# Kernel optimization log

Measured on AMD Instinct MI355X. Metric: run time of the kernel, lower is better.

The kernel has to match this reference:

```python
import jax, jax.numpy as jnp
import numpy as np

L = 2       # num_layers
D = 256     # d_model
DFF = 1024  # d_ffn
NH = 8      # n_heads
NP = 4      # n_points
CIN = 512   # in_channels
B = 8
HH = 64
WW = 64
EPS = 1e-5


def setup_inputs() -> dict:
    key = jax.random.key(0)
    ks = iter(jax.random.split(key, 48))
    def w(shape, s=0.02):
        return jax.random.normal(next(ks), shape, jnp.float32) * s
    inp = dict(
        x=jax.random.normal(next(ks), (B, CIN, HH, WW), jnp.float32),
        W_in=w((D, CIN)),
        bn1_g=jnp.ones((D,), jnp.float32), bn1_b=jnp.zeros((D,), jnp.float32),
        bn1_m=jnp.zeros((D,), jnp.float32), bn1_v=jnp.ones((D,), jnp.float32),
        query_embed=w((HH * WW, D), 1.0),
        Woff=w((L, D, NH * NP * 2)), boff=w((L, NH * NP * 2), 2.0),
        Wattn=w((L, D, NH * NP)), battn=jnp.zeros((L, NH * NP), jnp.float32),
        Wval=w((L, D, D)), bval=jnp.zeros((L, D), jnp.float32),
        Wo=w((L, D, D)), bo=jnp.zeros((L, D), jnp.float32),
        ln1_g=jnp.ones((L, D), jnp.float32), ln1_b=jnp.zeros((L, D), jnp.float32),
        W1=w((L, D, DFF)), b1=jnp.zeros((L, DFF), jnp.float32),
        W2=w((L, DFF, D)), b2=jnp.zeros((L, D), jnp.float32),
        ln2_g=jnp.ones((L, D), jnp.float32), ln2_b=jnp.zeros((L, D), jnp.float32),
        W_out=w((CIN, D)),
        bn2_g=jnp.ones((CIN,), jnp.float32), bn2_b=jnp.zeros((CIN,), jnp.float32),
        bn2_m=jnp.zeros((CIN,), jnp.float32), bn2_v=jnp.ones((CIN,), jnp.float32),
    )
    return inp


def layer_norm(x, g, b):
    m = jnp.mean(x, axis=-1, keepdims=True)
    v = jnp.mean((x - m) ** 2, axis=-1, keepdims=True)
    return (x - m) * jax.lax.rsqrt(v + EPS) * g + b


def bilinear_sample(value, loc, Hh, Ww):
    # value: (B, NH, dh, H*W); loc: (B, Lq, NH, NP, 2) normalized to [0,1]
    # Matches F.grid_sample(align_corners=False, padding_mode='zeros') with grid=2*loc-1.
    Bn, Lq, nH, P, _ = loc.shape
    gx = loc[..., 0] * Ww - 0.5
    gy = loc[..., 1] * Hh - 0.5
    x0 = jnp.floor(gx)
    y0 = jnp.floor(gy)
    wx = gx - x0
    wy = gy - y0
    x0i = x0.astype(jnp.int32)
    y0i = y0.astype(jnp.int32)

    def t(a):  # (B,Lq,NH,P) -> (B,NH,1,Lq*P)
        return jnp.transpose(a, (0, 2, 1, 3)).reshape(Bn, nH, 1, Lq * P)

    def gather(xi, yi):
        valid = (xi >= 0) & (xi < Ww) & (yi >= 0) & (yi < Hh)
        xc = jnp.clip(xi, 0, Ww - 1)
        yc = jnp.clip(yi, 0, Hh - 1)
        idx = t(yc * Ww + xc)  # (B,NH,1,Lq*P)
        v = jnp.take_along_axis(value, idx, axis=3)  # (B,NH,dh,Lq*P)
        return v * t(valid).astype(value.dtype)

    v00 = gather(x0i, y0i)
    v10 = gather(x0i + 1, y0i)
    v01 = gather(x0i, y0i + 1)
    v11 = gather(x0i + 1, y0i + 1)
    wxt = t(wx)
    wyt = t(wy)
    out = (v00 * (1 - wxt) * (1 - wyt) + v10 * wxt * (1 - wyt)
           + v01 * (1 - wxt) * wyt + v11 * wxt * wyt)
    return out.reshape(Bn, nH, -1, Lq, P)  # (B,NH,dh,Lq,NP)


def reference(x, W_in, bn1_g, bn1_b, bn1_m, bn1_v, query_embed,
              Woff, boff, Wattn, battn, Wval, bval, Wo, bo,
              ln1_g, ln1_b, W1, b1, W2, b2, ln2_g, ln2_b,
              W_out, bn2_g, bn2_b, bn2_m, bn2_v):
    Bn, C, Hh, Ww = x.shape
    HW = Hh * Ww
    dh = D // NH

    # proj_in: 1x1 conv (no bias) + BN (inference) + ReLU
    xp = jnp.einsum('bchw,dc->bdhw', x, W_in)
    xp = (xp - bn1_m[:, None, None]) * jax.lax.rsqrt(bn1_v[:, None, None] + EPS)
    xp = jax.nn.relu(xp * bn1_g[:, None, None] + bn1_b[:, None, None])
    src = xp.reshape(Bn, D, HW).transpose(0, 2, 1)  # (B, HW, D)

    # reference points: centers of pixels, normalized
    ry = (jnp.arange(Hh, dtype=jnp.float32) + 0.5) / Hh
    rx = (jnp.arange(Ww, dtype=jnp.float32) + 0.5) / Ww
    yy, xx = jnp.meshgrid(ry, rx, indexing='ij')
    refpts = jnp.stack([xx, yy], axis=-1).reshape(HW, 2)  # (HW, 2) as (x, y)
    norm = jnp.array([Ww, Hh], jnp.float32)

    q = jnp.broadcast_to(query_embed[None], (Bn, HW, D))
    for i in range(L):
        # --- MSDeformAttn (n_levels=1) ---
        val = (src @ Wval[i] + bval[i]).reshape(Bn, HW, NH, dh)
        val = val.transpose(0, 2, 3, 1)  # (B, NH, dh, HW)
        off = (q @ Woff[i] + boff[i]).reshape(Bn, HW, NH, NP, 2)
        attn = jax.nn.softmax((q @ Wattn[i] + battn[i]).reshape(Bn, HW, NH, NP), axis=-1)
        loc = refpts[None, :, None, None, :] + off / norm  # (B, HW, NH, NP, 2)
        samp = bilinear_sample(val, loc, Hh, Ww)  # (B, NH, dh, HW, NP)
        o = jnp.einsum('bhdqp,bhqp->bqhd', samp, attn.transpose(0, 2, 1, 3))
        o = o.reshape(Bn, HW, D) @ Wo[i] + bo[i]
        q = layer_norm(q + o, ln1_g[i], ln1_b[i])
        # --- FFN ---
        ffn = jax.nn.relu(q @ W1[i] + b1[i]) @ W2[i] + b2[i]
        q = layer_norm(q + ffn, ln2_g[i], ln2_b[i])

    # proj_out: 1x1 conv (no bias) + BN (inference) + ReLU
    y = q.transpose(0, 2, 1).reshape(Bn, D, Hh, Ww)
    y = jnp.einsum('bdhw,cd->bchw', y, W_out)
    y = (y - bn2_m[:, None, None]) * jax.lax.rsqrt(bn2_v[:, None, None] + EPS)
    return jax.nn.relu(y * bn2_g[:, None, None] + bn2_b[:, None, None])
```

## Files before the change

kernel.cpp:

```cpp
#include <hip/hip_runtime.h>
#include <cstdint>

#define LYR 2
#define DM  256
#define DFFN 1024
#define CINC 512
#define BBATCH 8
#define HWTOT 4096
#define EPSV 1e-5f

using u16 = unsigned short;
typedef __attribute__((ext_vector_type(8))) short bf16x8;
typedef __attribute__((ext_vector_type(4))) float f32x4;

__device__ inline u16 f2b(float v) {
    union { float f; uint32_t u; } x; x.f = v;
    uint32_t r = x.u + 0x7fffu + ((x.u >> 16) & 1u);
    return (u16)(r >> 16);
}
__device__ inline uint32_t pk2(float a, float b) {
    return (uint32_t)f2b(a) | ((uint32_t)f2b(b) << 16);
}
__device__ inline float blo(uint32_t d) {
    union { uint32_t i; float f; } x; x.i = d << 16; return x.f;
}
__device__ inline float bhi(uint32_t d) {
    union { uint32_t i; float f; } x; x.i = d & 0xffff0000u; return x.f;
}

template<int MODE>
__global__ __launch_bounds__(256) void mfma_gemm(
    const u16* __restrict__ A, const u16* __restrict__ Bt,
    const float* __restrict__ scale, const float* __restrict__ shift,
    void* __restrict__ Cv, int M, int N, int K, int ldc,
    long long a_zs, long long b_zs, long long c_zs, int swz, int gxlog)
{
    __shared__ u16 As[4][4096];
    __shared__ u16 Bs[4][4096];
    const int tid = threadIdx.x;
    const int lane = tid & 63;
    const int wid = tid >> 6;
    const int wm = (wid & 1) << 6, wn = (wid >> 1) << 6;
    const int quad = lane >> 4, r = lane & 15;

    int bx = blockIdx.x, by = blockIdx.y;
    if (swz) {
        int linear = by * gridDim.x + bx;
        int xcd = linear & 7;
        int s = linear >> 3;
        bx = s & (gridDim.x - 1);
        by = xcd * (gridDim.y >> 3) + (s >> gxlog);
    }
    const int m0 = by << 7, n0 = bx << 7;
    const u16* Ab = A + (long long)blockIdx.z * a_zs + (long long)m0 * K;
    const u16* Bb = Bt + (long long)blockIdx.z * b_zs + (long long)n0 * K;

    const int u0 = tid, u1 = tid + 256;
    const int mu0 = u0 >> 2, cu0 = (u0 & 3) ^ ((mu0 >> 1) & 3);
    const int mu1 = u1 >> 2, cu1 = (u1 & 3) ^ ((mu1 >> 1) & 3);
    const long long ga0 = (long long)mu0 * K + cu0 * 8;
    const long long ga1 = (long long)mu1 * K + cu1 * 8;

    int aoff[4], boff[4];
#pragma unroll
    for (int t = 0; t < 4; ++t) {
        int m = wm + t * 16 + r;
        aoff[t] = (m * 4 + (quad ^ ((m >> 1) & 3))) * 8;
        int n = wn + t * 16 + r;
        boff[t] = (n * 4 + (quad ^ ((n >> 1) & 3))) * 8;
    }

    f32x4 acc[4][4];
#pragma unroll
    for (int i = 0; i < 4; ++i)
#pragma unroll
        for (int j = 0; j < 4; ++j) acc[i][j] = (f32x4){0.f, 0.f, 0.f, 0.f};

    const int NT = K >> 5;

#define GSTAGE(g, b) do {                                                                       \
    const long long kk = (long long)(g) << 5;                                                   \
    __builtin_amdgcn_global_load_lds((const __attribute__((address_space(1))) void*)(Ab + ga0 + kk), \
        (__attribute__((address_space(3))) void*)(&As[b][u0 * 8]), 16, 0, 0);                   \
    __builtin_amdgcn_global_load_lds((const __attribute__((address_space(1))) void*)(Ab + ga1 + kk), \
        (__attribute__((address_space(3))) void*)(&As[b][u1 * 8]), 16, 0, 0);                   \
    __builtin_amdgcn_global_load_lds((const __attribute__((address_space(1))) void*)(Bb + ga0 + kk), \
        (__attribute__((address_space(3))) void*)(&Bs[b][u0 * 8]), 16, 0, 0);                   \
    __builtin_amdgcn_global_load_lds((const __attribute__((address_space(1))) void*)(Bb + ga1 + kk), \
        (__attribute__((address_space(3))) void*)(&Bs[b][u1 * 8]), 16, 0, 0);                   \
} while (0)

    GSTAGE(0, 0);
    GSTAGE(1, 1);
    GSTAGE(2, 2);

    for (int t = 0; t < NT; ++t) {
        if (t < NT - 2)       asm volatile("s_waitcnt vmcnt(8)" ::: "memory");
        else if (t == NT - 2) asm volatile("s_waitcnt vmcnt(4)" ::: "memory");
        else                  asm volatile("s_waitcnt vmcnt(0)" ::: "memory");
        __builtin_amdgcn_s_barrier();
        __builtin_amdgcn_sched_barrier(0);
        if (t + 3 < NT) GSTAGE(t + 3, (t + 3) & 3);
        const u16* Ap = As[t & 3];
        const u16* Bp = Bs[t & 3];
        bf16x8 af[4], bf[4];
#pragma unroll
        for (int tt = 0; tt < 4; ++tt) af[tt] = *(const bf16x8*)(Ap + aoff[tt]);
#pragma unroll
        for (int tt = 0; tt < 4; ++tt) bf[tt] = *(const bf16x8*)(Bp + boff[tt]);
#pragma unroll
        for (int i = 0; i < 4; ++i)
#pragma unroll
            for (int j = 0; j < 4; ++j)
                acc[i][j] = __builtin_amdgcn_mfma_f32_16x16x32_bf16(bf[j], af[i], acc[i][j], 0, 0, 0);
    }
#undef GSTAGE

    const long long zc = (long long)blockIdx.z * c_zs;
    float4 sh4[4], sc4[4];
    if (MODE != 3) {
#pragma unroll
        for (int j = 0; j < 4; ++j) {
            int colb = n0 + wn + j * 16 + quad * 4;
            sh4[j] = *(const float4*)&shift[colb];
            if (MODE == 1) sc4[j] = *(const float4*)&scale[colb];
        }
    }
#pragma unroll
    for (int i = 0; i < 4; ++i) {
        const int row = m0 + wm + i * 16 + r;
        float rsc = 0.f, rsh = 0.f;
        if (MODE == 3) { rsc = scale[row]; rsh = shift[row]; }
#pragma unroll
        for (int j = 0; j < 4; ++j) {
            const int colb = n0 + wn + j * 16 + quad * 4;
            f32x4 v = acc[i][j];
            if (MODE == 0) {
                uint2 o;
                o.x = pk2(v[0] + sh4[j].x, v[1] + sh4[j].y);
                o.y = pk2(v[2] + sh4[j].z, v[3] + sh4[j].w);
                *(uint2*)((u16*)Cv + zc + (long long)row * ldc + colb) = o;
            } else if (MODE == 1) {
                uint2 o;
                o.x = pk2(fmaxf(v[0] * sc4[j].x + sh4[j].x, 0.f), fmaxf(v[1] * sc4[j].y + sh4[j].y, 0.f));
                o.y = pk2(fmaxf(v[2] * sc4[j].z + sh4[j].z, 0.f), fmaxf(v[3] * sc4[j].w + sh4[j].w, 0.f));
                *(uint2*)((u16*)Cv + zc + (long long)row * ldc + colb) = o;
            } else if (MODE == 2) {
                float4 o = {v[0] + sh4[j].x, v[1] + sh4[j].y, v[2] + sh4[j].z, v[3] + sh4[j].w};
                *(float4*)((float*)Cv + zc + (long long)row * ldc + colb) = o;
            } else {
                float4 o = {fmaxf(v[0] * rsc + rsh, 0.f), fmaxf(v[1] * rsc + rsh, 0.f),
                            fmaxf(v[2] * rsc + rsh, 0.f), fmaxf(v[3] * rsc + rsh, 0.f)};
                *(float4*)((float*)Cv + zc + (long long)row * ldc + colb) = o;
            }
        }
    }
}

template<int WRITEQ, int OA>
__global__ __launch_bounds__(512, 4) void fused_layer(
    const u16* __restrict__ oms, const u16* __restrict__ woF,
    const u16* __restrict__ w1F, const u16* __restrict__ w2F,
    const u16* __restrict__ woaF,
    const float* __restrict__ bo, const float* __restrict__ b1, const float* __restrict__ b2,
    const float* __restrict__ boa1,
    float* __restrict__ q, u16* __restrict__ q16, float* __restrict__ offat,
    const float* __restrict__ g1, const float* __restrict__ be1,
    const float* __restrict__ g2, const float* __restrict__ be2)
{
    __shared__ u16 AqO[16384];
    __shared__ u16 AqQ[16384];
    __shared__ float red_s[8][64], red_ss[8][64];
    const int tid = threadIdx.x;
    const int lane = tid & 63;
    const int w = tid >> 6;
    const int quad = lane >> 4, r = lane & 15;
    const int m0 = blockIdx.x << 6;

    const u16* Ab = oms + (long long)m0 * DM;
#pragma unroll
    for (int i = 0; i < 4; ++i) {
        int u = tid + i * 512;
        int ks = u >> 8, v = u & 255;
        int m = v >> 2, c = (v & 3) ^ ((m >> 1) & 3);
        __builtin_amdgcn_global_load_lds((const __attribute__((address_space(1))) void*)(Ab + (long long)m * DM + ks * 32 + c * 8),
                                         (__attribute__((address_space(3))) void*)(AqO + u * 8), 16, 0, 0);
    }

    int aoff[4];
#pragma unroll
    for (int t = 0; t < 4; ++t) {
        int m = t * 16 + r;
        aoff[t] = (m * 4 + (quad ^ ((m >> 1) & 3))) * 8;
    }

    f32x4 acc[4][2];
#pragma unroll
    for (int i = 0; i < 4; ++i)
#pragma unroll
        for (int j = 0; j < 2; ++j) acc[i][j] = (f32x4){0.f, 0.f, 0.f, 0.f};

    __syncthreads();

#pragma unroll
    for (int ks = 0; ks < 8; ++ks) {
        const u16* bp = woF + ((size_t)(ks * 16 + 2 * w) * 64 + lane) * 8;
        bf16x8 bf0 = *(const bf16x8*)bp;
        bf16x8 bf1 = *(const bf16x8*)(bp + 512);
        bf16x8 af[4];
#pragma unroll
        for (int t = 0; t < 4; ++t) af[t] = *(const bf16x8*)(AqO + ks * 2048 + aoff[t]);
#pragma unroll
        for (int i = 0; i < 4; ++i) {
            acc[i][0] = __builtin_amdgcn_mfma_f32_16x16x32_bf16(bf0, af[i], acc[i][0], 0, 0, 0);
            acc[i][1] = __builtin_amdgcn_mfma_f32_16x16x32_bf16(bf1, af[i], acc[i][1], 0, 0, 0);
        }
    }

    float4 sh2[2];
#pragma unroll
    for (int j = 0; j < 2; ++j)
        sh2[j] = *(const float4*)&bo[w * 32 + j * 16 + quad * 4];

    float s_[4] = {0.f, 0.f, 0.f, 0.f}, ss_[4] = {0.f, 0.f, 0.f, 0.f};
#pragma unroll
    for (int i = 0; i < 4; ++i) {
        const int row = m0 + i * 16 + r;
#pragma unroll
        for (int j = 0; j < 2; ++j) {
            const int colb = w * 32 + j * 16 + quad * 4;
            float4 qo = *(const float4*)&q[(size_t)row * DM + colb];
            acc[i][j][0] += sh2[j].x + qo.x;
            acc[i][j][1] += sh2[j].y + qo.y;
            acc[i][j][2] += sh2[j].z + qo.z;
            acc[i][j][3] += sh2[j].w + qo.w;
#pragma unroll
            for (int e = 0; e < 4; ++e) {
                s_[i] += acc[i][j][e];
                ss_[i] += acc[i][j][e] * acc[i][j][e];
            }
        }
    }
#pragma unroll
    for (int i = 0; i < 4; ++i) {
        s_[i] += __shfl_xor(s_[i], 16);  ss_[i] += __shfl_xor(ss_[i], 16);
        s_[i] += __shfl_xor(s_[i], 32);  ss_[i] += __shfl_xor(ss_[i], 32);
    }
    if (quad == 0) {
#pragma unroll
        for (int i = 0; i < 4; ++i) {
            red_s[w][i * 16 + r] = s_[i];
            red_ss[w][i * 16 + r] = ss_[i];
        }
    }
    __syncthreads();

    float mean[4], rstd[4];
#pragma unroll
    for (int i = 0; i < 4; ++i) {
        float S = 0.f, SS = 0.f;
#pragma unroll
        for (int w2 = 0; w2 < 8; ++w2) { S += red_s[w2][i * 16 + r]; SS += red_ss[w2][i * 16 + r]; }
        mean[i] = S * (1.0f / 256.0f);
        rstd[i] = rsqrtf(SS * (1.0f / 256.0f) - mean[i] * mean[i] + EPSV);
    }

    f32x4 oreg[4][2];
    {
        float4 g4[2], bt4[2];
#pragma unroll
        for (int j = 0; j < 2; ++j) {
            int colb = w * 32 + j * 16 + quad * 4;
            g4[j] = *(const float4*)&g1[colb];
            bt4[j] = *(const float4*)&be1[colb];
        }
#pragma unroll
        for (int i = 0; i < 4; ++i) {
            const int mm = i * 16 + r;
#pragma unroll
            for (int j = 0; j < 2; ++j) {
                float o0 = (acc[i][j][0] - mean[i]) * rstd[i] * g4[j].x + bt4[j].x;
                float o1 = (acc[i][j][1] - mean[i]) * rstd[i] * g4[j].y + bt4[j].y;
                float o2 = (acc[i][j][2] - mean[i]) * rstd[i] * g4[j].z + bt4[j].z;
                float o3 = (acc[i][j][3] - mean[i]) * rstd[i] * g4[j].w + bt4[j].w;
                oreg[i][j] = (f32x4){o0, o1, o2, o3};
                const int pp = (j * 2 + (quad >> 1)) ^ ((r >> 1) & 3);
                *(uint2*)(AqQ + w * 2048 + (mm * 4 + pp) * 8 + (quad & 1) * 4) =
                    make_uint2(pk2(o0, o1), pk2(o2, o3));
            }
        }
    }
    __syncthreads();

    f32x4 acc2[4][2];
#pragma unroll
    for (int i = 0; i < 4; ++i)
#pragma unroll
        for (int j = 0; j < 2; ++j) acc2[i][j] = (f32x4){0.f, 0.f, 0.f, 0.f};

    for (int qq = 0; qq < 4; ++qq) {
        if (qq) __syncthreads();
#pragma unroll
        for (int j = 0; j < 2; ++j) {
            f32x4 a1[4];
#pragma unroll
            for (int i = 0; i < 4; ++i) a1[i] = (f32x4){0.f, 0.f, 0.f, 0.f};
            __builtin_amdgcn_s_setprio(1);
#pragma unroll
            for (int ks = 0; ks < 8; ++ks) {
                const u16* bp = w1F + ((size_t)(ks * 64 + qq * 16 + w * 2 + j) * 64 + lane) * 8;
                bf16x8 bf = *(const bf16x8*)bp;
                bf16x8 af[4];
#pragma unroll
                for (int t = 0; t < 4; ++t) af[t] = *(const bf16x8*)(AqQ + ks * 2048 + aoff[t]);
#pragma unroll
                for (int i = 0; i < 4; ++i)
                    a1[i] = __builtin_amdgcn_mfma_f32_16x16x32_bf16(bf, af[i], a1[i], 0, 0, 0);
            }
            __builtin_amdgcn_s_setprio(0);
            const int cb = qq * 256 + w * 32 + j * 16 + quad * 4;
            const float4 b14 = *(const float4*)&b1[cb];
            const int lane2 = r | (((j * 2 + (quad >> 1)) & 3) << 4);
            const int eo = (quad & 1) * 4;
#pragma unroll
            for (int i = 0; i < 4; ++i) {
                f32x4 v = a1[i];
                uint2 o;
                o.x = pk2(fmaxf(v[0] + b14.x, 0.f), fmaxf(v[1] + b14.y, 0.f));
                o.y = pk2(fmaxf(v[2] + b14.z, 0.f), fmaxf(v[3] + b14.w, 0.f));
                *(uint2*)(AqO + ((w * 4 + i) * 64 + lane2) * 8 + eo) = o;
            }
        }
        __syncthreads();

        __builtin_amdgcn_s_setprio(1);
#pragma unroll
        for (int ks = 0; ks < 8; ++ks) {
            const u16* bp = w2F + ((size_t)((qq * 8 + ks) * 16 + w * 2) * 64 + lane) * 8;
            bf16x8 bf0 = *(const bf16x8*)bp;
            bf16x8 bf1 = *(const bf16x8*)(bp + 512);
            bf16x8 af[4];
#pragma unroll
            for (int t = 0; t < 4; ++t) af[t] = *(const bf16x8*)(AqO + ((ks * 4 + t) * 64 + lane) * 8);
#pragma unroll
            for (int i = 0; i < 4; ++i) {
                acc2[i][0] = __builtin_amdgcn_mfma_f32_16x16x32_bf16(bf0, af[i], acc2[i][0], 0, 0, 0);
                acc2[i][1] = __builtin_amdgcn_mfma_f32_16x16x32_bf16(bf1, af[i], acc2[i][1], 0, 0, 0);
            }
        }
        __builtin_amdgcn_s_setprio(0);
    }

#pragma unroll
    for (int j = 0; j < 2; ++j)
        sh2[j] = *(const float4*)&b2[w * 32 + j * 16 + quad * 4];

#pragma unroll
    for (int i = 0; i < 4; ++i) { s_[i] = 0.f; ss_[i] = 0.f; }
#pragma unroll
    for (int i = 0; i < 4; ++i) {
#pragma unroll
        for (int j = 0; j < 2; ++j) {
            acc2[i][j][0] += sh2[j].x + oreg[i][j][0];
            acc2[i][j][1] += sh2[j].y + oreg[i][j][1];
            acc2[i][j][2] += sh2[j].z + oreg[i][j][2];
            acc2[i][j][3] += sh2[j].w + oreg[i][j][3];
#pragma unroll
            for (int e = 0; e < 4; ++e) {
                s_[i] += acc2[i][j][e];
                ss_[i] += acc2[i][j][e] * acc2[i][j][e];
            }
        }
    }
#pragma unroll
    for (int i = 0; i < 4; ++i) {
        s_[i] += __shfl_xor(s_[i], 16);  ss_[i] += __shfl_xor(ss_[i], 16);
        s_[i] += __shfl_xor(s_[i], 32);  ss_[i] += __shfl_xor(ss_[i], 32);
    }
    if (quad == 0) {
#pragma unroll
        for (int i = 0; i < 4; ++i) {
            red_s[w][i * 16 + r] = s_[i];
            red_ss[w][i * 16 + r] = ss_[i];
        }
    }
    __syncthreads();

#pragma unroll
    for (int i = 0; i < 4; ++i) {
        float S = 0.f, SS = 0.f;
#pragma unroll
        for (int w2 = 0; w2 < 8; ++w2) { S += red_s[w2][i * 16 + r]; SS += red_ss[w2][i * 16 + r]; }
        mean[i] = S * (1.0f / 256.0f);
        rstd[i] = rsqrtf(SS * (1.0f / 256.0f) - mean[i] * mean[i] + EPSV);
    }

    float4 g4[2], bt4[2];
#pragma unroll
    for (int j = 0; j < 2; ++j) {
        int colb = w * 32 + j * 16 + quad * 4;
        g4[j] = *(const float4*)&g2[colb];
        bt4[j] = *(const float4*)&be2[colb];
    }
#pragma unroll
    for (int i = 0; i < 4; ++i) {
        const int row = m0 + i * 16 + r;
#pragma unroll
        for (int j = 0; j < 2; ++j) {
            const int colb = w * 32 + j * 16 + quad * 4;
            float o0 = (acc2[i][j][0] - mean[i]) * rstd[i] * g4[j].x + bt4[j].x;
            float o1 = (acc2[i][j][1] - mean[i]) * rstd[i] * g4[j].y + bt4[j].y;
            float o2 = (acc2[i][j][2] - mean[i]) * rstd[i] * g4[j].z + bt4[j].z;
            float o3 = (acc2[i][j][3] - mean[i]) * rstd[i] * g4[j].w + bt4[j].w;
            oreg[i][j] = (f32x4){o0, o1, o2, o3};
            if (WRITEQ)
                *(float4*)&q[(size_t)row * DM + colb] = make_float4(o0, o1, o2, o3);
            *(uint2*)(q16 + (size_t)row * DM + colb) = make_uint2(pk2(o0, o1), pk2(o2, o3));
        }
    }

    if (OA) {
#pragma unroll
        for (int i = 0; i < 4; ++i) {
            const int mm = i * 16 + r;
#pragma unroll
            for (int j = 0; j < 2; ++j) {
                const int pp = (j * 2 + (quad >> 1)) ^ ((r >> 1) & 3);
                *(uint2*)(AqQ + w * 2048 + (mm * 4 + pp) * 8 + (quad & 1) * 4) =
                    make_uint2(pk2(oreg[i][j][0], oreg[i][j][1]),
                               pk2(oreg[i][j][2], oreg[i][j][3]));
            }
        }
        __syncthreads();
        f32x4 aoa[4];
#pragma unroll
        for (int i = 0; i < 4; ++i) aoa[i] = (f32x4){0.f, 0.f, 0.f, 0.f};
#pragma unroll
        for (int ks = 0; ks < 8; ++ks) {
            const u16* bp = woaF + ((size_t)(ks * 8 + w) * 64 + lane) * 8;
            bf16x8 bf = *(const bf16x8*)bp;
            bf16x8 af[4];
#pragma unroll
            for (int t = 0; t < 4; ++t) af[t] = *(const bf16x8*)(AqQ + ks * 2048 + aoff[t]);
#pragma unroll
            for (int i = 0; i < 4; ++i)
                aoa[i] = __builtin_amdgcn_mfma_f32_16x16x32_bf16(bf, af[i], aoa[i], 0, 0, 0);
        }
        const float4 bo4 = *(const float4*)&boa1[w * 16 + quad * 4];
#pragma unroll
        for (int i = 0; i < 4; ++i) {
            const int row = m0 + i * 16 + r;
            float4 o = {aoa[i][0] + bo4.x, aoa[i][1] + bo4.y, aoa[i][2] + bo4.z, aoa[i][3] + bo4.w};
            *(float4*)&offat[(size_t)row * 128 + w * 16 + quad * 4] = o;
        }
    }
}

__device__ __attribute__((noinline)) void tconv(const float* src, u16* dst, int K, int N, int tk, int tn)
{
    __shared__ float t[32][33];
    const int tx = threadIdx.x & 31, ty = threadIdx.x >> 5;
#pragma unroll
    for (int i = 0; i < 4; ++i)
        t[ty + i * 8][tx] = src[(size_t)(tk * 32 + ty + i * 8) * N + tn * 32 + tx];
    __syncthreads();
#pragma unroll
    for (int i = 0; i < 4; ++i)
        dst[(size_t)(tn * 32 + ty + i * 8) * K + tk * 32 + tx] = f2b(t[tx][ty + i * 8]);
}

__device__ __attribute__((noinline)) void tconv_oa(const float* Woff, const float* Wattn, u16* dst, int tk, int tn)
{
    __shared__ float t[32][33];
    const int tx = threadIdx.x & 31, ty = threadIdx.x >> 5;
#pragma unroll
    for (int i = 0; i < 4; ++i) {
        int k = tk * 32 + ty + i * 8, n = tn * 32 + tx;
        float v = (n < 64) ? Woff[k * 64 + n] : ((n < 96) ? Wattn[k * 32 + n - 64] : 0.f);
        t[ty + i * 8][tx] = v;
    }
    __syncthreads();
#pragma unroll
    for (int i = 0; i < 4; ++i)
        dst[(size_t)(tn * 32 + ty + i * 8) * 256 + tk * 32 + tx] = f2b(t[tx][ty + i * 8]);
}

__device__ __attribute__((noinline)) void frag_prep(const float* W, u16* dst, int ks, int nc, int N)
{
    __shared__ float t[32][256];
    const int tid = threadIdx.x;
#pragma unroll
    for (int kk = 0; kk < 32; ++kk)
        t[kk][tid] = W[(size_t)(ks * 32 + kk) * N + nc * 256 + tid];
    __syncthreads();
    const int NT16 = N >> 4;
#pragma unroll
    for (int i = 0; i < 4; ++i) {
        int idx = tid + i * 256;
        int nt = idx >> 6, l = idx & 63;
        int n = nt * 16 + (l & 15);
        int kb = (l >> 4) * 8;
        u16 o[8];
#pragma unroll
        for (int e = 0; e < 8; ++e) o[e] = f2b(t[kb + e][n]);
        *(uint4*)(dst + ((size_t)(ks * NT16 + nc * 16 + nt) * 64 + l) * 8) = *(const uint4*)o;
    }
}

__device__ __attribute__((noinline)) void frag_prep_oa(const float* Woff, const float* Wattn, u16* dst, int ks)
{
    __shared__ float t[32][128];
    const int tid = threadIdx.x;
#pragma unroll
    for (int kk2 = 0; kk2 < 16; ++kk2) {
        int idx = tid + kk2 * 256;
        int row = idx >> 7, col = idx & 127;
        float v = (col < 64) ? Woff[(size_t)(ks * 32 + row) * 64 + col]
                 : ((col < 96) ? Wattn[(size_t)(ks * 32 + row) * 32 + col - 64] : 0.f);
        t[row][col] = v;
    }
    __syncthreads();
#pragma unroll
    for (int u2 = 0; u2 < 2; ++u2) {
        int unit = tid + u2 * 256;
        int nt = unit >> 6, l = unit & 63;
        int n = nt * 16 + (l & 15);
        int kb = (l >> 4) * 8;
        u16 o[8];
#pragma unroll
        for (int e = 0; e < 8; ++e) o[e] = f2b(t[kb + e][n]);
        *(uint4*)(dst + ((size_t)(ks * 8 + nt) * 64 + l) * 8) = *(const uint4*)o;
    }
}

__global__ __launch_bounds__(256) void prep_weights(
    const float* __restrict__ Wval, const float* __restrict__ Wo,
    const float* __restrict__ W1, const float* __restrict__ W2,
    const float* __restrict__ Woff, const float* __restrict__ Wattn,
    const float* __restrict__ boff, const float* __restrict__ battn,
    const float* __restrict__ W_in, const float* __restrict__ W_out,
    const float* __restrict__ bn1g, const float* __restrict__ bn1b,
    const float* __restrict__ bn1m, const float* __restrict__ bn1v,
    const float* __restrict__ bn2g, const float* __restrict__ bn2b,
    const float* __restrict__ bn2m, const float* __restrict__ bn2v,
    u16* __restrict__ wvalT, u16* __restrict__ woF, u16* __restrict__ w1F,
    u16* __restrict__ w2F, u16* __restrict__ woaT, u16* __restrict__ woaF,
    u16* __restrict__ winC, u16* __restrict__ woutC,
    float* __restrict__ bn1sc, float* __restrict__ bn1sh,
    float* __restrict__ bn2sc, float* __restrict__ bn2sh, float* __restrict__ boa)
{
    int bid = blockIdx.x;
    if (bid < 128) {
        int l = bid >> 6, r2 = bid & 63;
        tconv(Wval + l * 65536, wvalT + l * 65536, 256, 256, r2 & 7, r2 >> 3);
    } else if (bid < 160) {
        int r2 = bid - 128;
        tconv_oa(Woff, Wattn, woaT, r2 & 7, r2 >> 3);
    } else if (bid < 176) {
        int i2 = bid - 160;
        frag_prep(Wo + (i2 >> 3) * 65536, woF + (i2 >> 3) * 65536, i2 & 7, 0, 256);
    } else if (bid < 240) {
        int i2 = bid - 176, l = i2 >> 5, r2 = i2 & 31;
        frag_prep(W1 + l * 262144, w1F + l * 262144, r2 >> 2, r2 & 3, 1024);
    } else if (bid < 304) {
        int i2 = bid - 240;
        frag_prep(W2 + (i2 >> 5) * 262144, w2F + (i2 >> 5) * 262144, i2 & 31, 0, 256);
    } else if (bid < 312) {
        frag_prep_oa(Woff + 16384, Wattn + 8192, woaF, bid - 304);
    } else if (bid < 344) {
        int g2 = bid - 312, base = g2 * 4096, t = threadIdx.x;
#pragma unroll
        for (int k = 0; k < 16; ++k) winC[base + k * 256 + t] = f2b(W_in[base + k * 256 + t]);
    } else if (bid < 376) {
        int g2 = bid - 344, base = g2 * 4096, t = threadIdx.x;
#pragma unroll
        for (int k = 0; k < 16; ++k) woutC[base + k * 256 + t] = f2b(W_out[base + k * 256 + t]);
    } else {
        int t = threadIdx.x;
        { float s = bn1g[t] * rsqrtf(bn1v[t] + EPSV); bn1sc[t] = s; bn1sh[t] = bn1b[t] - bn1m[t] * s; }
        for (int c = 0; c < 2; ++c) {
            int i = c * 256 + t;
            float s = bn2g[i] * rsqrtf(bn2v[i] + EPSV);
            bn2sc[i] = s; bn2sh[i] = bn2b[i] - bn2m[i] * s;
        }
        if (t < 128)
            for (int l = 0; l < 2; ++l)
                boa[l * 128 + t] = (t < 64) ? boff[l * 64 + t]
                                 : ((t < 96) ? battn[l * 32 + t - 64] : 0.f);
    }
}

__global__ __launch_bounds__(256) void transpose_x(const float* __restrict__ x, u16* __restrict__ xT)
{
    __shared__ float t[64][65];
    const int b = blockIdx.z, p0 = blockIdx.y << 6, c0 = blockIdx.x << 6;
    const int tx = threadIdx.x & 63, ty = threadIdx.x >> 6;
    const float* xb = x + ((size_t)b * CINC + c0) * HWTOT + p0;
#pragma unroll
    for (int i = 0; i < 16; ++i)
        t[ty + i * 4][tx] = xb[(size_t)(ty + i * 4) * HWTOT + tx];
    __syncthreads();
    u16* xo = xT + ((size_t)b * HWTOT + p0) * CINC + c0;
#pragma unroll
    for (int i = 0; i < 16; ++i)
        xo[(size_t)(ty + i * 4) * CINC + tx] = f2b(t[tx][ty + i * 4]);
}

struct IW { int eo; float w; };

__global__ __launch_bounds__(256) void sample_kernel(
    const u16* __restrict__ val,
    const float* __restrict__ oa,
    u16* __restrict__ oms,
    int lofs, unsigned int mask)
{
    __shared__ float s_oa[8][96];
    __shared__ IW s_iw[8][32][5];
    const int t = threadIdx.x;
    const int bq0 = blockIdx.x << 3;
    const int b = blockIdx.x >> 9;

    {
        int qi = t >> 5, j = t & 31;
        if (j < 24)
            ((float4*)s_oa[qi])[j] = ((const float4*)oa)[((size_t)((bq0 + qi) & mask)) * 32 + j];
    }
    __syncthreads();

    {
        const int qi = t >> 5, hp = t & 31, h = hp >> 2, p = hp & 3;
        const float* so = s_oa[qi];
        float l0 = so[64 + h * 4 + 0], l1 = so[64 + h * 4 + 1];
        float l2 = so[64 + h * 4 + 2], l3 = so[64 + h * 4 + 3];
        float mx = fmaxf(fmaxf(l0, l1), fmaxf(l2, l3));
        float e0 = __expf(l0 - mx), e1 = __expf(l1 - mx), e2 = __expf(l2 - mx), e3 = __expf(l3 - mx);
        float inv = 1.0f / (e0 + e1 + e2 + e3);
        float aw = ((p == 0) ? e0 : (p == 1) ? e1 : (p == 2) ? e2 : e3) * inv;
        const int bq = bq0 + qi;
        float gx = (float)(bq & 63) + so[hp * 2 + 0];
        float gy = (float)((bq >> 6) & 63) + so[hp * 2 + 1];
        float x0f = floorf(gx), y0f = floorf(gy);
        float wx = gx - x0f, wy = gy - y0f;
        int x0 = (int)x0f, y0 = (int)y0f;
#pragma unroll
        for (int c = 0; c < 4; ++c) {
            int xi = x0 + (c & 1), yi = y0 + (c >> 1);
            bool ok = (xi >= 0) && (xi < 64) && (yi >= 0) && (yi < 64);
            float wgt = ((c & 1) ? wx : 1.0f - wx) * ((c >> 1) ? wy : 1.0f - wy);
            s_iw[qi][hp][c].eo = ok ? ((yi * 64 + xi) << 9) : 0;
            s_iw[qi][hp][c].w = ok ? aw * wgt : 0.f;
        }
    }
    __syncthreads();

    {
        const int qi = t >> 5, l = t & 31, h = l >> 2, cc = l & 3;
        const u16* base = val + ((size_t)b << 21) + lofs + (h << 5) + (cc << 3);
        float a[8] = {0.f, 0.f, 0.f, 0.f, 0.f, 0.f, 0.f, 0.f};
#pragma unroll
        for (int p = 0; p < 4; ++p)
#pragma unroll
            for (int c = 0; c < 4; ++c) {
                IW iw = s_iw[qi][(h << 2) + p][c];
                uint4 v = *(const uint4*)(base + iw.eo);
                a[0] += iw.w * blo(v.x); a[1] += iw.w * bhi(v.x);
                a[2] += iw.w * blo(v.y); a[3] += iw.w * bhi(v.y);
                a[4] += iw.w * blo(v.z); a[5] += iw.w * bhi(v.z);
                a[6] += iw.w * blo(v.w); a[7] += iw.w * bhi(v.w);
            }
        uint4 o;
        o.x = (uint32_t)f2b(a[0]) | ((uint32_t)f2b(a[1]) << 16);
        o.y = (uint32_t)f2b(a[2]) | ((uint32_t)f2b(a[3]) << 16);
        o.z = (uint32_t)f2b(a[4]) | ((uint32_t)f2b(a[5]) << 16);
        o.w = (uint32_t)f2b(a[6]) | ((uint32_t)f2b(a[7]) << 16);
        *(uint4*)(oms + (size_t)(bq0 + qi) * 256 + (h << 5) + (cc << 3)) = o;
    }
}

__global__ __launch_bounds__(256) void bcast_q(
    const float4* __restrict__ qe, float4* __restrict__ q, u16* __restrict__ q16)
{
    const int i = blockIdx.x * 256 + threadIdx.x;
    float4 v = qe[i];
    uint2 pk = make_uint2(pk2(v.x, v.y), pk2(v.z, v.w));
#pragma unroll
    for (int b = 0; b < BBATCH; ++b)
        q[(size_t)b * 262144 + i] = v;
    ((uint2*)q16)[i] = pk;
}

extern "C" void kernel_launch(void* const* d_in, const int* in_sizes, int n_in,
                              void* d_out, int out_size, void* d_ws, size_t ws_size,
                              hipStream_t stream)
{
    (void)in_sizes; (void)n_in; (void)out_size; (void)ws_size;
    const float* x     = (const float*)d_in[0];
    const float* W_in  = (const float*)d_in[1];
    const float* bn1_g = (const float*)d_in[2];
    const float* bn1_b = (const float*)d_in[3];
    const float* bn1_m = (const float*)d_in[4];
    const float* bn1_v = (const float*)d_in[5];
    const float* qe    = (const float*)d_in[6];
    const float* Woff  = (const float*)d_in[7];
    const float* boff  = (const float*)d_in[8];
    const float* Wattn = (const float*)d_in[9];
    const float* battn = (const float*)d_in[10];
    const float* Wval  = (const float*)d_in[11];
    const float* bval  = (const float*)d_in[12];
    const float* Wo    = (const float*)d_in[13];
    const float* bo    = (const float*)d_in[14];
    const float* ln1_g = (const float*)d_in[15];
    const float* ln1_b = (const float*)d_in[16];
    const float* W1    = (const float*)d_in[17];
    const float* b1    = (const float*)d_in[18];
    const float* W2    = (const float*)d_in[19];
    const float* b2    = (const float*)d_in[20];
    const float* ln2_g = (const float*)d_in[21];
    const float* ln2_b = (const float*)d_in[22];
    const float* W_out = (const float*)d_in[23];
    const float* bn2_g = (const float*)d_in[24];
    const float* bn2_b = (const float*)d_in[25];
    const float* bn2_m = (const float*)d_in[26];
    const float* bn2_v = (const float*)d_in[27];
    float* out = (float*)d_out;

    char* w = (char*)d_ws;
    char* pool    = w;          w += 67108864;
    float* q      = (float*)w;  w += 33554432;
    u16*  q16     = (u16*)w;    w += 16777216;
    u16*  src16   = (u16*)w;    w += 16777216;
    u16*  wvalT   = (u16*)w;    w += 262144;
    u16*  woF     = (u16*)w;    w += 262144;
    u16*  w1F     = (u16*)w;    w += 1048576;
    u16*  w2F     = (u16*)w;    w += 1048576;
    u16*  woaT    = (u16*)w;    w += 65536;
    u16*  woaF    = (u16*)w;    w += 65536;
    u16*  winC    = (u16*)w;    w += 262144;
    u16*  woutC   = (u16*)w;    w += 262144;
    float* bn1sc  = (float*)w;  w += 1024;
    float* bn1sh  = (float*)w;  w += 1024;
    float* bn2sc  = (float*)w;  w += 2048;
    float* bn2sh  = (float*)w;  w += 2048;
    float* boa    = (float*)w;  w += 1024;

    u16*  xT     = (u16*)pool;
    u16*  val16  = (u16*)pool;
    float* offat = (float*)(pool + 33554432);
    u16*  oms16  = (u16*)(pool + 50331648);

    prep_weights<<<dim3(377), 256, 0, stream>>>(
        Wval, Wo, W1, W2, Woff, Wattn, boff, battn, W_in, W_out,
        bn1_g, bn1_b, bn1_m, bn1_v, bn2_g, bn2_b, bn2_m, bn2_v,
        wvalT, woF, w1F, w2F, woaT, woaF, winC, woutC, bn1sc, bn1sh, bn2sc, bn2sh, boa);
    transpose_x<<<dim3(CINC / 64, HWTOT / 64, BBATCH), 256, 0, stream>>>(x, xT);
    bcast_q<<<dim3(1024), 256, 0, stream>>>((const float4*)qe, (float4*)q, q16);

    mfma_gemm<1><<<dim3(2, 256, 1), 256, 0, stream>>>(
        xT, winC, bn1sc, bn1sh, src16, 32768, 256, 512, 256, 0, 0, 0, 1, 1);

    mfma_gemm<2><<<dim3(1, 32, 1), 256, 0, stream>>>(
        q16, woaT, nullptr, boa, offat, 4096, 128, 256, 128, 0, 0, 0, 1, 0);

    mfma_gemm<0><<<dim3(4, 256, 1), 256, 0, stream>>>(
        src16, wvalT, nullptr, bval, val16, 32768, 512, 256, 512, 0, 0, 0, 1, 2);

    sample_kernel<<<dim3(4096), 256, 0, stream>>>(val16, offat, oms16, 0, 4095u);
    fused_layer<1, 1><<<dim3(512), 512, 0, stream>>>(
        oms16, woF, w1F, w2F, woaF, bo, b1, b2, boa + 128, q, q16, offat,
        ln1_g, ln1_b, ln2_g, ln2_b);

    sample_kernel<<<dim3(4096), 256, 0, stream>>>(val16, offat, oms16, 256, 0xFFFFFFFFu);
    fused_layer<0, 0><<<dim3(512), 512, 0, stream>>>(
        oms16, woF + 65536, w1F + 262144, w2F + 262144, nullptr,
        bo + 256, b1 + 1024, b2 + 256, nullptr, q, q16, nullptr,
        ln1_g + 256, ln1_b + 256, ln2_g + 256, ln2_b + 256);

    mfma_gemm<3><<<dim3(32, 4, BBATCH), 256, 0, stream>>>(
        woutC, q16, bn2sc, bn2sh, out, 512, 4096, 256, 4096,
        0, (long long)HWTOT * DM, (long long)CINC * HWTOT, 0, 0);
}
```

Before: 451.2 us.

## Add full-N GEMM kernel for input and value projections, drop q broadcast

Adds a gemm_fullN kernel in which each 512-thread block owns 64 rows and computes all output columns. The block streams A through a 3-stage LDS ring via global_load_lds and reads B weights directly from global memory in pre-swizzled MFMA fragment layout, so A tiles are no longer re-read once per column block. The input projection and the value projection use this kernel, with new weight fragment-prep routines. The fp32 query broadcast to 8 batches is removed; the first fused layer reads the residual directly from query_embed. The cost is higher register pressure and reliance on B fragments being served from L2.

```diff
diff --git a/kernel.cpp b/kernel.cpp
--- a/kernel.cpp
+++ b/kernel.cpp
@@ -117,13 +117,12 @@
 #undef GSTAGE
 
     const long long zc = (long long)blockIdx.z * c_zs;
-    float4 sh4[4], sc4[4];
+    float4 sh4[4];
     if (MODE != 3) {
 #pragma unroll
         for (int j = 0; j < 4; ++j) {
             int colb = n0 + wn + j * 16 + quad * 4;
             sh4[j] = *(const float4*)&shift[colb];
-            if (MODE == 1) sc4[j] = *(const float4*)&scale[colb];
         }
     }
 #pragma unroll
@@ -135,17 +134,7 @@
         for (int j = 0; j < 4; ++j) {
             const int colb = n0 + wn + j * 16 + quad * 4;
             f32x4 v = acc[i][j];
-            if (MODE == 0) {
-                uint2 o;
-                o.x = pk2(v[0] + sh4[j].x, v[1] + sh4[j].y);
-                o.y = pk2(v[2] + sh4[j].z, v[3] + sh4[j].w);
-                *(uint2*)((u16*)Cv + zc + (long long)row * ldc + colb) = o;
-            } else if (MODE == 1) {
-                uint2 o;
-                o.x = pk2(fmaxf(v[0] * sc4[j].x + sh4[j].x, 0.f), fmaxf(v[1] * sc4[j].y + sh4[j].y, 0.f));
-                o.y = pk2(fmaxf(v[2] * sc4[j].z + sh4[j].z, 0.f), fmaxf(v[3] * sc4[j].w + sh4[j].w, 0.f));
-                *(uint2*)((u16*)Cv + zc + (long long)row * ldc + colb) = o;
-            } else if (MODE == 2) {
+            if (MODE == 2) {
                 float4 o = {v[0] + sh4[j].x, v[1] + sh4[j].y, v[2] + sh4[j].z, v[3] + sh4[j].w};
                 *(float4*)((float*)Cv + zc + (long long)row * ldc + colb) = o;
             } else {
@@ -157,14 +146,126 @@
     }
 }
 
-template<int WRITEQ, int OA>
+template<int NTW, int NT, int MODE>
+__global__ __launch_bounds__(512, 3) void gemm_fullN(
+    const u16* __restrict__ A, const u16* __restrict__ Bf,
+    const float* __restrict__ scale, const float* __restrict__ shift,
+    u16* __restrict__ out, int ldc, long long lstr)
+{
+    constexpr int K = NT * 32;
+    __shared__ u16 As[3][2048];
+    const int tid = threadIdx.x;
+    const int lane = tid & 63;
+    const int w = tid >> 6;
+    const int quad = lane >> 4, r = lane & 15;
+    const int m0 = blockIdx.x << 6;
+    const u16* Ab = A + (long long)m0 * K;
+
+    const int mA = tid >> 2, cA = (tid & 3) ^ ((mA >> 1) & 3);
+    const long long gaA = (long long)mA * K + cA * 8;
+    const bool stager = tid < 256;
+
+    int aoff[4];
+#pragma unroll
+    for (int t = 0; t < 4; ++t) {
+        int m = t * 16 + r;
+        aoff[t] = (m * 4 + (quad ^ ((m >> 1) & 3))) * 8;
+    }
+
+    size_t bbase[NTW];
+#pragma unroll
+    for (int t = 0; t < NTW; ++t) {
+        int g = w * NTW + t;
+        bbase[t] = (size_t)(g >> 4) * lstr + ((size_t)(g & 15) * 64 + lane) * 8;
+    }
+
+    f32x4 acc[4][NTW];
+#pragma unroll
+    for (int i = 0; i < 4; ++i)
+#pragma unroll
+        for (int t = 0; t < NTW; ++t) acc[i][t] = (f32x4){0.f, 0.f, 0.f, 0.f};
+
+    if (stager) {
+        __builtin_amdgcn_global_load_lds((const __attribute__((address_space(1))) void*)(Ab + gaA),
+                                         (__attribute__((address_space(3))) void*)(&As[0][tid * 8]), 16, 0, 0);
+        __builtin_amdgcn_global_load_lds((const __attribute__((address_space(1))) void*)(Ab + gaA + 32),
+                                         (__attribute__((address_space(3))) void*)(&As[1][tid * 8]), 16, 0, 0);
+    }
+    __builtin_amdgcn_sched_barrier(0);
+    bf16x8 bc[NTW];
+#pragma unroll
+    for (int t = 0; t < NTW; ++t) bc[t] = *(const bf16x8*)(Bf + bbase[t]);
+
+    int cb = 0;
+    for (int t = 0; t < NT; ++t) {
+        if constexpr (NTW == 2) asm volatile("s_waitcnt vmcnt(3)" ::: "memory");
+        else                    asm volatile("s_waitcnt vmcnt(5)" ::: "memory");
+        __builtin_amdgcn_s_barrier();
+        __builtin_amdgcn_sched_barrier(0);
+        int nb = cb + 2; if (nb >= 3) nb -= 3;
+        if (stager && t + 2 < NT)
+            __builtin_amdgcn_global_load_lds((const __attribute__((address_space(1))) void*)(Ab + gaA + (long long)(t + 2) * 32),
+                                             (__attribute__((address_space(3))) void*)(&As[nb][tid * 8]), 16, 0, 0);
+        bf16x8 bn[NTW];
+        if (t + 1 < NT) {
+#pragma unroll
+            for (int tt = 0; tt < NTW; ++tt)
+                bn[tt] = *(const bf16x8*)(Bf + bbase[tt] + (size_t)(t + 1) * 8192);
+        } else {
+#pragma unroll
+            for (int tt = 0; tt < NTW; ++tt) bn[tt] = bc[tt];
+        }
+
+        const u16* Ac = As[cb];
+        bf16x8 af[4];
+#pragma unroll
+        for (int tt = 0; tt < 4; ++tt) af[tt] = *(const bf16x8*)(Ac + aoff[tt]);
+#pragma unroll
+        for (int i = 0; i < 4; ++i)
+#pragma unroll
+            for (int tt = 0; tt < NTW; ++tt)
+                acc[i][tt] = __builtin_amdgcn_mfma_f32_16x16x32_bf16(bc[tt], af[i], acc[i][tt], 0, 0, 0);
+#pragma unroll
+        for (int tt = 0; tt < NTW; ++tt) bc[tt] = bn[tt];
+        cb = (cb + 1 == 3) ? 0 : cb + 1;
+    }
+
+    float4 sh4[NTW], sc4[NTW];
+#pragma unroll
+    for (int tt = 0; tt < NTW; ++tt) {
+        int colg = (w * NTW + tt) * 16 + quad * 4;
+        sh4[tt] = *(const float4*)&shift[colg];
+        if (MODE == 1) sc4[tt] = *(const float4*)&scale[colg];
+    }
+#pragma unroll
+    for (int i = 0; i < 4; ++i) {
+        const int row = m0 + i * 16 + r;
+#pragma unroll
+        for (int tt = 0; tt < NTW; ++tt) {
+            const int colg = (w * NTW + tt) * 16 + quad * 4;
+            f32x4 v = acc[i][tt];
+            uint2 o;
+            if (MODE == 1) {
+                o.x = pk2(fmaxf(v[0] * sc4[tt].x + sh4[tt].x, 0.f), fmaxf(v[1] * sc4[tt].y + sh4[tt].y, 0.f));
+                o.y = pk2(fmaxf(v[2] * sc4[tt].z + sh4[tt].z, 0.f), fmaxf(v[3] * sc4[tt].w + sh4[tt].w, 0.f));
+            } else {
+                o.x = pk2(v[0] + sh4[tt].x, v[1] + sh4[tt].y);
+                o.y = pk2(v[2] + sh4[tt].z, v[3] + sh4[tt].w);
+            }
+            *(uint2*)(out + (size_t)row * ldc + colg) = o;
+        }
+    }
+}
+
+template<int WRITEQ, int OA, int QE>
 __global__ __launch_bounds__(512, 4) void fused_layer(
     const u16* __restrict__ oms, const u16* __restrict__ woF,
     const u16* __restrict__ w1F, const u16* __restrict__ w2F,
     const u16* __restrict__ woaF,
     const float* __restrict__ bo, const float* __restrict__ b1, const float* __restrict__ b2,
     const float* __restrict__ boa1,
-    float* __restrict__ q, u16* __restrict__ q16, float* __restrict__ offat,
+    const float* __restrict__ qe, float* __restrict__ q, u16* __restrict__ q16,
+    float* __restrict__ offat,
     const float* __restrict__ g1, const float* __restrict__ be1,
     const float* __restrict__ g2, const float* __restrict__ be2)
 {
@@ -229,7 +330,8 @@
 #pragma unroll
         for (int j = 0; j < 2; ++j) {
             const int colb = w * 32 + j * 16 + quad * 4;
-            float4 qo = *(const float4*)&q[(size_t)row * DM + colb];
+            float4 qo = QE ? *(const float4*)&qe[(size_t)(row & 4095) * DM + colb]
+                           : *(const float4*)&q[(size_t)row * DM + colb];
             acc[i][j][0] += sh2[j].x + qo.x;
             acc[i][j][1] += sh2[j].y + qo.y;
             acc[i][j][2] += sh2[j].z + qo.z;
@@ -456,19 +558,6 @@
     }
 }
 
-__device__ __attribute__((noinline)) void tconv(const float* src, u16* dst, int K, int N, int tk, int tn)
-{
-    __shared__ float t[32][33];
-    const int tx = threadIdx.x & 31, ty = threadIdx.x >> 5;
-#pragma unroll
-    for (int i = 0; i < 4; ++i)
-        t[ty + i * 8][tx] = src[(size_t)(tk * 32 + ty + i * 8) * N + tn * 32 + tx];
-    __syncthreads();
-#pragma unroll
-    for (int i = 0; i < 4; ++i)
-        dst[(size_t)(tn * 32 + ty + i * 8) * K + tk * 32 + tx] = f2b(t[tx][ty + i * 8]);
-}
-
 __device__ __attribute__((noinline)) void tconv_oa(const float* Woff, const float* Wattn, u16* dst, int tk, int tn)
 {
     __shared__ float t[32][33];
@@ -504,6 +593,27 @@
 #pragma unroll
         for (int e = 0; e < 8; ++e) o[e] = f2b(t[kb + e][n]);
         *(uint4*)(dst + ((size_t)(ks * NT16 + nc * 16 + nt) * 64 + l) * 8) = *(const uint4*)o;
+    }
+}
+
+__device__ __attribute__((noinline)) void frag_prep_t(const float* W, u16* dst, int ks)
+{
+    __shared__ float t[32][256];
+    const int tid = threadIdx.x;
+#pragma unroll
+    for (int kk = 0; kk < 32; ++kk)
+        t[kk][tid] = W[(size_t)tid * 512 + ks * 32 + kk];
+    __syncthreads();
+#pragma unroll
+    for (int i = 0; i < 4; ++i) {
+        int idx = tid + i * 256;
+        int nt = idx >> 6, l = idx & 63;
+        int n = nt * 16 + (l & 15);
+        int kb = (l >> 4) * 8;
+        u16 o[8];
+#pragma unroll
+        for (int e = 0; e < 8; ++e) o[e] = f2b(t[kb + e][n]);
+        *(uint4*)(dst + ((size_t)(ks * 16 + nt) * 64 + l) * 8) = *(const uint4*)o;
     }
 }
 
@@ -543,36 +653,34 @@
     const float* __restrict__ bn1m, const float* __restrict__ bn1v,
     const float* __restrict__ bn2g, const float* __restrict__ bn2b,
     const float* __restrict__ bn2m, const float* __restrict__ bn2v,
-    u16* __restrict__ wvalT, u16* __restrict__ woF, u16* __restrict__ w1F,
+    u16* __restrict__ wvalF, u16* __restrict__ woF, u16* __restrict__ w1F,
     u16* __restrict__ w2F, u16* __restrict__ woaT, u16* __restrict__ woaF,
-    u16* __restrict__ winC, u16* __restrict__ woutC,
+    u16* __restrict__ winF, u16* __restrict__ woutC,
     float* __restrict__ bn1sc, float* __restrict__ bn1sh,
     float* __restrict__ bn2sc, float* __restrict__ bn2sh, float* __restrict__ boa)
 {
     int bid = blockIdx.x;
-    if (bid < 128) {
-        int l = bid >> 6, r2 = bid & 63;
-        tconv(Wval + l * 65536, wvalT + l * 65536, 256, 256, r2 & 7, r2 >> 3);
-    } else if (bid < 160) {
-        int r2 = bid - 128;
+    if (bid < 16) {
+        int l = bid >> 3, ks = bid & 7;
+        frag_prep(Wval + l * 65536, wvalF + l * 65536, ks, 0, 256);
+    } else if (bid < 48) {
+        int r2 = bid - 16;
         tconv_oa(Woff, Wattn, woaT, r2 & 7, r2 >> 3);
-    } else if (bid < 176) {
-        int i2 = bid - 160;
+    } else if (bid < 64) {
+        int i2 = bid - 48;
         frag_prep(Wo + (i2 >> 3) * 65536, woF + (i2 >> 3) * 65536, i2 & 7, 0, 256);
-    } else if (bid < 240) {
-        int i2 = bid - 176, l = i2 >> 5, r2 = i2 & 31;
+    } else if (bid < 128) {
+        int i2 = bid - 64, l = i2 >> 5, r2 = i2 & 31;
         frag_prep(W1 + l * 262144, w1F + l * 262144, r2 >> 2, r2 & 3, 1024);
-    } else if (bid < 304) {
-        int i2 = bid - 240;
+    } else if (bid < 192) {
+        int i2 = bid - 128;
         frag_prep(W2 + (i2 >> 5) * 262144, w2F + (i2 >> 5) * 262144, i2 & 31, 0, 256);
-    } else if (bid < 312) {
-        frag_prep_oa(Woff + 16384, Wattn + 8192, woaF, bid - 304);
-    } else if (bid < 344) {
-        int g2 = bid - 312, base = g2 * 4096, t = threadIdx.x;
-#pragma unroll
-        for (int k = 0; k < 16; ++k) winC[base + k * 256 + t] = f2b(W_in[base + k * 256 + t]);
-    } else if (bid < 376) {
-        int g2 = bid - 344, base = g2 * 4096, t = threadIdx.x;
+    } else if (bid < 200) {
+        frag_prep_oa(Woff + 16384, Wattn + 8192, woaF, bid - 192);
+    } else if (bid < 216) {
+        frag_prep_t(W_in, winF, bid - 200);
+    } else if (bid < 248) {
+        int g2 = bid - 216, base = g2 * 4096, t = threadIdx.x;
 #pragma unroll
         for (int k = 0; k < 16; ++k) woutC[base + k * 256 + t] = f2b(W_out[base + k * 256 + t]);
     } else {
@@ -678,15 +786,11 @@
 }
 
 __global__ __launch_bounds__(256) void bcast_q(
-    const float4* __restrict__ qe, float4* __restrict__ q, u16* __restrict__ q16)
+    const float4* __restrict__ qe, u16* __restrict__ q16)
 {
     const int i = blockIdx.x * 256 + threadIdx.x;
     float4 v = qe[i];
-    uint2 pk = make_uint2(pk2(v.x, v.y), pk2(v.z, v.w));
-#pragma unroll
-    for (int b = 0; b < BBATCH; ++b)
-        q[(size_t)b * 262144 + i] = v;
-    ((uint2*)q16)[i] = pk;
+    ((uint2*)q16)[i] = make_uint2(pk2(v.x, v.y), pk2(v.z, v.w));
 }
 
 extern "C" void kernel_launch(void* const* d_in, const int* in_sizes, int n_in,
@@ -729,13 +833,13 @@
     float* q      = (float*)w;  w += 33554432;
     u16*  q16     = (u16*)w;    w += 16777216;
     u16*  src16   = (u16*)w;    w += 16777216;
-    u16*  wvalT   = (u16*)w;    w += 262144;
+    u16*  wvalF   = (u16*)w;    w += 262144;
     u16*  woF     = (u16*)w;    w += 262144;
     u16*  w1F     = (u16*)w;    w += 1048576;
     u16*  w2F     = (u16*)w;    w += 1048576;
     u16*  woaT    = (u16*)w;    w += 65536;
     u16*  woaF    = (u16*)w;    w += 65536;
-    u16*  winC    = (u16*)w;    w += 262144;
+    u16*  winF    = (u16*)w;    w += 262144;
     u16*  woutC   = (u16*)w;    w += 262144;
     float* bn1sc  = (float*)w;  w += 1024;
     float* bn1sh  = (float*)w;  w += 1024;
@@ -748,31 +852,31 @@
     float* offat = (float*)(pool + 33554432);
     u16*  oms16  = (u16*)(pool + 50331648);
 
-    prep_weights<<<dim3(377), 256, 0, stream>>>(
+    prep_weights<<<dim3(249), 256, 0, stream>>>(
         Wval, Wo, W1, W2, Woff, Wattn, boff, battn, W_in, W_out,
         bn1_g, bn1_b, bn1_m, bn1_v, bn2_g, bn2_b, bn2_m, bn2_v,
-        wvalT, woF, w1F, w2F, woaT, woaF, winC, woutC, bn1sc, bn1sh, bn2sc, bn2sh, boa);
+        wvalF, woF, w1F, w2F, woaT, woaF, winF, woutC, bn1sc, bn1sh, bn2sc, bn2sh, boa);
     transpose_x<<<dim3(CINC / 64, HWTOT / 64, BBATCH), 256, 0, stream>>>(x, xT);
-    bcast_q<<<dim3(1024), 256, 0, stream>>>((const float4*)qe, (float4*)q, q16);
-
-    mfma_gemm<1><<<dim3(2, 256, 1), 256, 0, stream>>>(
-        xT, winC, bn1sc, bn1sh, src16, 32768, 256, 512, 256, 0, 0, 0, 1, 1);
+    bcast_q<<<dim3(1024), 256, 0, stream>>>((const float4*)qe, q16);
+
+    gemm_fullN<2, 16, 1><<<dim3(512), 512, 0, stream>>>(
+        xT, winF, bn1sc, bn1sh, src16, 256, 0);
 
     mfma_gemm<2><<<dim3(1, 32, 1), 256, 0, stream>>>(
         q16, woaT, nullptr, boa, offat, 4096, 128, 256, 128, 0, 0, 0, 1, 0);
 
-    mfma_gemm<0><<<dim3(4, 256, 1), 256, 0, stream>>>(
-        src16, wvalT, nullptr, bval, val16, 32768, 512, 256, 512, 0, 0, 0, 1, 2);
+    gemm_fullN<4, 8, 0><<<dim3(512), 512, 0, stream>>>(
+        src16, wvalF, nullptr, bval, val16, 512, 65536);
 
     sample_kernel<<<dim3(4096), 256, 0, stream>>>(val16, offat, oms16, 0, 4095u);
-    fused_layer<1, 1><<<dim3(512), 512, 0, stream>>>(
-        oms16, woF, w1F, w2F, woaF, bo, b1, b2, boa + 128, q, q16, offat,
+    fused_layer<1, 1, 1><<<dim3(512), 512, 0, stream>>>(
+        oms16, woF, w1F, w2F, woaF, bo, b1, b2, boa + 128, qe, q, q16, offat,
         ln1_g, ln1_b, ln2_g, ln2_b);
 
     sample_kernel<<<dim3(4096), 256, 0, stream>>>(val16, offat, oms16, 256, 0xFFFFFFFFu);
-    fused_layer<0, 0><<<dim3(512), 512, 0, stream>>>(
+    fused_layer<0, 0, 0><<<dim3(512), 512, 0, stream>>>(
         oms16, woF + 65536, w1F + 262144, w2F + 262144, nullptr,
-        bo + 256, b1 + 1024, b2 + 256, nullptr, q, q16, nullptr,
+        bo + 256, b1 + 1024, b2 + 256, nullptr, nullptr, q, q16, nullptr,
         ln1_g + 256, ln1_b + 256, ln2_g + 256, ln2_b + 256);
 
     mfma_gemm<3><<<dim3(32, 4, BBATCH), 256, 0, stream>>>(
```

After: 424.6 us (median of 2 runs). 1.06x faster.
